# Optimization experiments

Hardware: AMD Instinct MI355X
Metric: run time of the kernel (lower is better)

Reference implementation:

```python
import jax, jax.numpy as jnp
import numpy as np
import itertools

B, T, D, H, E, K = 2, 1024, 768, 3072, 8, 2


def _trigram_dirs():
    # 8 vertices of the cube {-1,+1}^3, L2-normalized rows (matches F.normalize)
    t = np.array(list(itertools.product([-1.0, 1.0], repeat=3)), dtype=np.float32)[:E]
    t = t / np.linalg.norm(t, axis=1, keepdims=True)
    return jnp.asarray(t)


def setup_inputs() -> dict:
    key = jax.random.key(0)
    k1, k2, k3, k4 = jax.random.split(key, 4)
    x = jax.random.normal(k1, (B, T, D), jnp.float32)
    Wr = jax.random.normal(k2, (3, D), jnp.float32) * 0.02
    W1 = jax.random.normal(k3, (E, D, H), jnp.float32) * 0.02
    W2 = jax.random.normal(k4, (E, H, D), jnp.float32) * 0.02
    return {"x": x, "Wr": Wr, "W1": W1, "W2": W2}


def reference(x, Wr, W1, W2):
    Bb, Tt, Dd = x.shape
    xf = x.reshape(-1, Dd)                       # (N, D)
    dirs = _trigram_dirs()                       # (E, 3)
    z3 = xf @ Wr.T                               # (N, 3)
    logits = z3 @ dirs.T                         # (N, E)
    probs = jax.nn.softmax(logits, axis=-1)
    topv, topi = jax.lax.top_k(probs, K)         # (N, K)
    topv = topv / topv.sum(axis=-1, keepdims=True)
    N = xf.shape[0]
    # dense gate matrix: gates[n, e] = sum_k topv[n,k] * [topi[n,k]==e]
    gates = jnp.zeros((N, E), xf.dtype).at[jnp.arange(N)[:, None], topi].add(topv)
    # dense-all-experts equivalent of the masked gather/scatter loop
    h = jax.nn.gelu(jnp.einsum('nd,edh->neh', xf, W1), approximate=False)
    y = jnp.einsum('neh,ehd->ned', h, W2)
    out = jnp.einsum('ne,ned->nd', gates, y).reshape(Bb, Tt, Dd)
    tokens_per_expert = probs.mean(axis=0)
    aux_loss = 0.01 * jnp.mean((tokens_per_expert - 1.0 / E) ** 2)
    return out, aux_loss
```

## Files before the change

### kernel.cpp

```cpp
#include <hip/hip_runtime.h>
#include <hip/hip_bf16.h>
#include <math.h>

#define DD 768
#define HH 3072
#define EE 8
#define NN 2048
#define PP 5120
#define PT 40

typedef __attribute__((ext_vector_type(8))) short short8;
typedef __attribute__((ext_vector_type(4))) float floatx4;

typedef const __attribute__((address_space(1))) void gas_void;
typedef __attribute__((address_space(3))) void las_void;

__device__ __forceinline__ void gld16(const void* g, void* l) {
    __builtin_amdgcn_global_load_lds((gas_void*)g, (las_void*)l, 16, 0, 0);
}

__device__ __forceinline__ unsigned short f2bf(float f) {
    union { float f; unsigned int u; } v; v.f = f;
    unsigned int u = v.u;
    u += 0x7fffu + ((u >> 16) & 1u);
    return (unsigned short)(u >> 16);
}

__global__ __launch_bounds__(256) void routing_kernel(
    const float* __restrict__ x, const float* __restrict__ Wr,
    int* __restrict__ counts, float* __restrict__ psum,
    int* __restrict__ top_e, float* __restrict__ top_g)
{
    __shared__ float wr[3 * DD];
    __shared__ float lpsum[EE];
    int tid = threadIdx.x;
    for (int i = tid; i < 3 * DD; i += 256) wr[i] = Wr[i];
    if (tid < EE) lpsum[tid] = 0.f;
    __syncthreads();

    int sub = tid & 15;
    int n = blockIdx.x * 16 + (tid >> 4);
    const float* xr = x + (size_t)n * DD;
    float z0 = 0.f, z1 = 0.f, z2 = 0.f;
#pragma unroll
    for (int i = 0; i < DD / 64; i++) {
        int d = i * 64 + sub * 4;
        float4 v = *(const float4*)(xr + d);
        z0 = fmaf(v.x, wr[d], z0);         z0 = fmaf(v.y, wr[d+1], z0);
        z0 = fmaf(v.z, wr[d+2], z0);       z0 = fmaf(v.w, wr[d+3], z0);
        z1 = fmaf(v.x, wr[DD+d], z1);      z1 = fmaf(v.y, wr[DD+d+1], z1);
        z1 = fmaf(v.z, wr[DD+d+2], z1);    z1 = fmaf(v.w, wr[DD+d+3], z1);
        z2 = fmaf(v.x, wr[2*DD+d], z2);    z2 = fmaf(v.y, wr[2*DD+d+1], z2);
        z2 = fmaf(v.z, wr[2*DD+d+2], z2);  z2 = fmaf(v.w, wr[2*DD+d+3], z2);
    }
#pragma unroll
    for (int m = 8; m; m >>= 1) {
        z0 += __shfl_xor(z0, m, 16);
        z1 += __shfl_xor(z1, m, 16);
        z2 += __shfl_xor(z2, m, 16);
    }

    if (sub == 0) {
        const float r3 = 0.57735026918962576f;
        float p[EE];
        float mx = -1e30f;
#pragma unroll
        for (int e = 0; e < EE; e++) {
            float s0 = (e & 4) ? z0 : -z0;
            float s1 = (e & 2) ? z1 : -z1;
            float s2 = (e & 1) ? z2 : -z2;
            p[e] = (s0 + s1 + s2) * r3;
            mx = fmaxf(mx, p[e]);
        }
        float sum = 0.f;
#pragma unroll
        for (int e = 0; e < EE; e++) { p[e] = expf(p[e] - mx); sum += p[e]; }
        float inv_s = 1.f / sum;
#pragma unroll
        for (int e = 0; e < EE; e++) p[e] *= inv_s;

        int e1 = 0; float p1 = p[0];
#pragma unroll
        for (int e = 1; e < EE; e++) if (p[e] > p1) { p1 = p[e]; e1 = e; }
        int e2 = -1; float p2 = -1.f;
#pragma unroll
        for (int e = 0; e < EE; e++) if (e != e1 && p[e] > p2) { p2 = p[e]; e2 = e; }
        float inv_t = 1.f / (p1 + p2);
        top_e[2*n]   = e1;  top_g[2*n]   = p1 * inv_t;
        top_e[2*n+1] = e2;  top_g[2*n+1] = p2 * inv_t;
        atomicAdd(&counts[e1], 1);
        atomicAdd(&counts[e2], 1);
#pragma unroll
        for (int e = 0; e < EE; e++) atomicAdd(&lpsum[e], p[e]);
    }
    __syncthreads();
    if (tid < EE) atomicAdd(&psum[tid], lpsum[tid]);
}

__global__ void scan_aux_kernel(const int* __restrict__ counts, const float* __restrict__ psum,
                                int* __restrict__ cursor, int* __restrict__ poffs,
                                float* __restrict__ out_aux)
{
    if (threadIdx.x == 0) {
        int run = 0;
        for (int e = 0; e < EE; e++) {
            poffs[e] = run;
            cursor[e] = run;
            run += ((counts[e] + 127) >> 7) << 7;
        }
        poffs[EE] = run;
        float s = 0.f;
        for (int e = 0; e < EE; e++) {
            float t = psum[e] * (1.f / NN) - (1.f / EE);
            s += t * t;
        }
        *out_aux = 0.01f * (s * (1.f / EE));
    }
}

__global__ __launch_bounds__(256) void scatter_kernel(
    const int* __restrict__ top_e, int* __restrict__ cursor,
    int* __restrict__ row_tok, int* __restrict__ inv_row)
{
    int n = blockIdx.x * 256 + threadIdx.x;
#pragma unroll
    for (int k = 0; k < 2; k++) {
        int e = top_e[2*n + k];
        int pos = atomicAdd(&cursor[e], 1);
        row_tok[pos]    = n;
        inv_row[2*n+k]  = pos;
    }
}

__global__ __launch_bounds__(192) void gather_cast_kernel(
    const float* __restrict__ x, const int* __restrict__ counts,
    const int* __restrict__ poffs, const int* __restrict__ row_tok,
    unsigned short* __restrict__ xg)
{
    int t = threadIdx.x;
    int pr = blockIdx.x * 4 + t / 48;
    int c0 = (t % 48) * 16;
    int e = 0;
#pragma unroll
    for (int i = 0; i < EE - 1; i++) if (pr >= poffs[i + 1]) e = i + 1;
    int local = pr - poffs[e];
    unsigned short* dst = xg + (size_t)pr * DD + c0;
    if (local < counts[e]) {
        int tok = row_tok[pr];
        const float4* sp = (const float4*)(x + (size_t)tok * DD + c0);
        alignas(16) unsigned short tmp[16];
#pragma unroll
        for (int j = 0; j < 4; j++) {
            float4 v = sp[j];
            tmp[4*j+0] = f2bf(v.x); tmp[4*j+1] = f2bf(v.y);
            tmp[4*j+2] = f2bf(v.z); tmp[4*j+3] = f2bf(v.w);
        }
        *(uint4*)dst       = *(uint4*)&tmp[0];
        *(uint4*)(dst + 8) = *(uint4*)&tmp[8];
    } else {
        uint4 z = {0, 0, 0, 0};
        *(uint4*)dst       = z;
        *(uint4*)(dst + 8) = z;
    }
}

__global__ __launch_bounds__(256) void transpose_cast_kernel(
    const float* __restrict__ W1, const float* __restrict__ W2,
    unsigned short* __restrict__ w1t, unsigned short* __restrict__ w2t)
{
    int z = blockIdx.z, e = blockIdx.y, bx = blockIdx.x;
    const float* src; unsigned short* dst; int R, C, SC;
    if (z == 0) { R = DD; C = HH; SC = 12; src = W1 + (size_t)e * R * C; dst = w1t + (size_t)e * R * C; }
    else        { R = HH; C = DD; SC = 3;  src = W2 + (size_t)e * R * C; dst = w2t + (size_t)e * R * C; }
    int rt = bx / SC, cs = bx % SC;
    int r0 = rt * 64, cbase = cs * 256;

    __shared__ unsigned short tile[64][66];
    int tid = threadIdx.x;
    int lr = tid >> 2, lc = (tid & 3) * 16;
    int oc = tid >> 2, orr = (tid & 3) * 16;
    const float* srow = src + (size_t)(r0 + lr) * C + cbase + lc;

    float4 v[16];
#pragma unroll
    for (int i = 0; i < 4; i++) {
        const float4* sp = (const float4*)(srow + i * 64);
#pragma unroll
        for (int j = 0; j < 4; j++) v[i * 4 + j] = sp[j];
    }
#pragma unroll
    for (int i = 0; i < 16; i++)
        asm volatile("" :: "v"(v[i].x), "v"(v[i].y), "v"(v[i].z), "v"(v[i].w));

#pragma unroll
    for (int i = 0; i < 4; i++) {
        if (i) __syncthreads();
#pragma unroll
        for (int j = 0; j < 4; j++) {
            float4 t = v[i * 4 + j];
            tile[lr][lc + 4*j + 0] = f2bf(t.x);
            tile[lr][lc + 4*j + 1] = f2bf(t.y);
            tile[lr][lc + 4*j + 2] = f2bf(t.z);
            tile[lr][lc + 4*j + 3] = f2bf(t.w);
        }
        __syncthreads();
        alignas(16) unsigned short tmp[16];
#pragma unroll
        for (int j = 0; j < 16; j++) tmp[j] = tile[orr + j][oc];
        unsigned short* dp = dst + (size_t)(cbase + i * 64 + oc) * R + r0 + orr;
        *(uint4*)dp       = *(uint4*)&tmp[0];
        *(uint4*)(dp + 8) = *(uint4*)&tmp[8];
    }
}

__global__ __launch_bounds__(256) void gemm1_kernel(
    const unsigned short* __restrict__ xg, const unsigned short* __restrict__ w1t,
    unsigned short* __restrict__ h, const int* __restrict__ poffs)
{
    int t = blockIdx.x;
    if (t * 128 >= poffs[EE]) return;
    int e = 0;
#pragma unroll
    for (int i = 0; i < EE - 1; i++) if (t * 128 >= poffs[i + 1]) e = i + 1;
    int row0 = t * 128, n0 = blockIdx.y * 128;

    __shared__ alignas(16) unsigned short As[2][128][32];
    __shared__ alignas(16) unsigned short Bs[2][128][32];

    int tid = threadIdx.x;
    int w = tid >> 6, lane = tid & 63;
    int quad = lane >> 4, l15 = lane & 15;
    int wm = (w & 1) * 64, wn = (w >> 1) * 64;

    const unsigned short* abase = xg + (size_t)row0 * DD;
    const unsigned short* bbase = w1t + (size_t)e * HH * DD + (size_t)n0 * DD;

    int c0 = w * 64 + lane, c1 = 256 + c0;
    const unsigned short* ga0 = abase + (c0 >> 2) * DD + (c0 & 3) * 8;
    const unsigned short* ga1 = abase + (c1 >> 2) * DD + (c1 & 3) * 8;
    const unsigned short* gb0 = bbase + (c0 >> 2) * DD + (c0 & 3) * 8;
    const unsigned short* gb1 = bbase + (c1 >> 2) * DD + (c1 & 3) * 8;
    int lofs0 = (w * 64) * 8;
    int lofs1 = (256 + w * 64) * 8;

    floatx4 acc[4][4];
#pragma unroll
    for (int i = 0; i < 4; i++)
#pragma unroll
        for (int j = 0; j < 4; j++)
#pragma unroll
            for (int r = 0; r < 4; r++) acc[i][j][r] = 0.f;

    const int NT = DD / 32;
    gld16(ga0, &As[0][0][0] + lofs0);
    gld16(ga1, &As[0][0][0] + lofs1);
    gld16(gb0, &Bs[0][0][0] + lofs0);
    gld16(gb1, &Bs[0][0][0] + lofs1);
    __syncthreads();

    for (int kt = 0; kt < NT; kt++) {
        int cur = kt & 1;
        if (kt + 1 < NT) {
            int k0 = (kt + 1) * 32;
            unsigned short* nA = &As[cur ^ 1][0][0];
            unsigned short* nB = &Bs[cur ^ 1][0][0];
            gld16(ga0 + k0, nA + lofs0);
            gld16(ga1 + k0, nA + lofs1);
            gld16(gb0 + k0, nB + lofs0);
            gld16(gb1 + k0, nB + lofs1);
        }
        short8 afr[4], bfr[4];
#pragma unroll
        for (int fm = 0; fm < 4; fm++) afr[fm] = *(const short8*)&As[cur][wm + fm*16 + l15][quad * 8];
#pragma unroll
        for (int fn = 0; fn < 4; fn++) bfr[fn] = *(const short8*)&Bs[cur][wn + fn*16 + l15][quad * 8];
#pragma unroll
        for (int fm = 0; fm < 4; fm++)
#pragma unroll
            for (int fn = 0; fn < 4; fn++)
                acc[fm][fn] = __builtin_amdgcn_mfma_f32_16x16x32_bf16(afr[fm], bfr[fn], acc[fm][fn], 0, 0, 0);
        __syncthreads();
    }

#pragma unroll
    for (int fm = 0; fm < 4; fm++)
#pragma unroll
        for (int r = 0; r < 4; r++) {
            int rt = wm + fm * 16 + quad * 4 + r;
            size_t hrow = (size_t)(row0 + rt) * HH;
#pragma unroll
            for (int fn = 0; fn < 4; fn++) {
                int col = n0 + wn + fn * 16 + l15;
                float v = acc[fm][fn][r];
                float g = 0.5f * v * (1.f + erff(v * 0.70710678118654752f));
                h[hrow + col] = f2bf(g);
            }
        }
}

__global__ __launch_bounds__(256) void gemm2_kernel(
    const unsigned short* __restrict__ h, const unsigned short* __restrict__ w2t,
    float* __restrict__ ybuf, const int* __restrict__ poffs)
{
    int t = blockIdx.x;
    if (t * 128 >= poffs[EE]) return;
    int e = 0;
#pragma unroll
    for (int i = 0; i < EE - 1; i++) if (t * 128 >= poffs[i + 1]) e = i + 1;
    int row0 = t * 128, n0 = blockIdx.y * 128;
    int kz = blockIdx.z;

    __shared__ alignas(16) unsigned short As[2][128][32];
    __shared__ alignas(16) unsigned short Bs[2][128][32];

    int tid = threadIdx.x;
    int w = tid >> 6, lane = tid & 63;
    int quad = lane >> 4, l15 = lane & 15;
    int wm = (w & 1) * 64, wn = (w >> 1) * 64;

    const unsigned short* abase = h + (size_t)row0 * HH + kz * (HH / 2);
    const unsigned short* bbase = w2t + (size_t)e * DD * HH + (size_t)n0 * HH + kz * (HH / 2);

    int c0 = w * 64 + lane, c1 = 256 + c0;
    const unsigned short* ga0 = abase + (c0 >> 2) * HH + (c0 & 3) * 8;
    const unsigned short* ga1 = abase + (c1 >> 2) * HH + (c1 & 3) * 8;
    const unsigned short* gb0 = bbase + (c0 >> 2) * HH + (c0 & 3) * 8;
    const unsigned short* gb1 = bbase + (c1 >> 2) * HH + (c1 & 3) * 8;
    int lofs0 = (w * 64) * 8;
    int lofs1 = (256 + w * 64) * 8;

    floatx4 acc[4][4];
#pragma unroll
    for (int i = 0; i < 4; i++)
#pragma unroll
        for (int j = 0; j < 4; j++)
#pragma unroll
            for (int r = 0; r < 4; r++) acc[i][j][r] = 0.f;

    const int NT = (HH / 2) / 32;
    gld16(ga0, &As[0][0][0] + lofs0);
    gld16(ga1, &As[0][0][0] + lofs1);
    gld16(gb0, &Bs[0][0][0] + lofs0);
    gld16(gb1, &Bs[0][0][0] + lofs1);
    __syncthreads();

    for (int kt = 0; kt < NT; kt++) {
        int cur = kt & 1;
        if (kt + 1 < NT) {
            int k0 = (kt + 1) * 32;
            unsigned short* nA = &As[cur ^ 1][0][0];
            unsigned short* nB = &Bs[cur ^ 1][0][0];
            gld16(ga0 + k0, nA + lofs0);
            gld16(ga1 + k0, nA + lofs1);
            gld16(gb0 + k0, nB + lofs0);
            gld16(gb1 + k0, nB + lofs1);
        }
        short8 afr[4], bfr[4];
#pragma unroll
        for (int fm = 0; fm < 4; fm++) afr[fm] = *(const short8*)&As[cur][wm + fm*16 + l15][quad * 8];
#pragma unroll
        for (int fn = 0; fn < 4; fn++) bfr[fn] = *(const short8*)&Bs[cur][wn + fn*16 + l15][quad * 8];
#pragma unroll
        for (int fm = 0; fm < 4; fm++)
#pragma unroll
            for (int fn = 0; fn < 4; fn++)
                acc[fm][fn] = __builtin_amdgcn_mfma_f32_16x16x32_bf16(afr[fm], bfr[fn], acc[fm][fn], 0, 0, 0);
        __syncthreads();
    }

    float* yb = ybuf + (size_t)kz * PP * DD + (size_t)row0 * DD;
#pragma unroll
    for (int fm = 0; fm < 4; fm++)
#pragma unroll
        for (int r = 0; r < 4; r++) {
            int rt = wm + fm * 16 + quad * 4 + r;
            float* op = yb + (size_t)rt * DD + n0 + wn;
#pragma unroll
            for (int fn = 0; fn < 4; fn++)
                op[fn * 16 + l15] = acc[fm][fn][r];
        }
}

__global__ __launch_bounds__(192) void combine_kernel(
    const float* __restrict__ ybuf, const int* __restrict__ inv_row,
    const float* __restrict__ top_g, float* __restrict__ out)
{
    int n = blockIdx.x;
    int c = threadIdx.x * 4;
    int r0 = inv_row[2*n], r1 = inv_row[2*n+1];
    float g0 = top_g[2*n], g1 = top_g[2*n+1];
    const size_t S = (size_t)PP * DD;
    const float* y0 = ybuf + (size_t)r0 * DD + c;
    const float* y1 = ybuf + (size_t)r1 * DD + c;
    float4 a0 = *(const float4*)y0, b0 = *(const float4*)(y0 + S);
    float4 a1 = *(const float4*)y1, b1 = *(const float4*)(y1 + S);
    float4 o;
    o.x = g0 * (a0.x + b0.x) + g1 * (a1.x + b1.x);
    o.y = g0 * (a0.y + b0.y) + g1 * (a1.y + b1.y);
    o.z = g0 * (a0.z + b0.z) + g1 * (a1.z + b1.z);
    o.w = g0 * (a0.w + b0.w) + g1 * (a1.w + b1.w);
    *(float4*)(out + (size_t)n * DD + c) = o;
}

extern "C" void kernel_launch(void* const* d_in, const int* in_sizes, int n_in,
                              void* d_out, int out_size, void* d_ws, size_t ws_size,
                              hipStream_t stream)
{
    const float* x  = (const float*)d_in[0];
    const float* Wr = (const float*)d_in[1];
    const float* W1 = (const float*)d_in[2];
    const float* W2 = (const float*)d_in[3];
    float* out = (float*)d_out;

    char* ws = (char*)d_ws;
    int*   counts   = (int*)(ws + 0);
    int*   cursor   = (int*)(ws + 32);
    float* psum     = (float*)(ws + 64);
    int*   poffs    = (int*)(ws + 96);
    int*   top_e    = (int*)(ws + 1024);
    float* top_g    = (float*)(ws + 1024 + 16384);
    int*   row_tok  = (int*)(ws + 1024 + 2 * 16384);
    int*   inv_row  = (int*)(ws + 1024 + 2 * 16384 + PP * 4);
    size_t off = (size_t)(1024 + 2 * 16384 + PP * 4 + 16384 + 255) & ~(size_t)255;
    unsigned short* xg  = (unsigned short*)(ws + off); off += (size_t)PP * DD * 2;
    unsigned short* hbf = (unsigned short*)(ws + off); off += (size_t)PP * HH * 2;
    unsigned short* w1t = (unsigned short*)(ws + off); off += (size_t)EE * DD * HH * 2;
    unsigned short* w2t = (unsigned short*)(ws + off);
    float* ybuf = (float*)w1t;

    hipMemsetAsync(ws, 0, 96, stream);

    transpose_cast_kernel<<<dim3(144, EE, 2), 256, 0, stream>>>(W1, W2, w1t, w2t);
    routing_kernel<<<dim3(NN / 16), 256, 0, stream>>>(x, Wr, counts, psum, top_e, top_g);
    scan_aux_kernel<<<1, 64, 0, stream>>>(counts, psum, cursor, poffs, out + (size_t)NN * DD);
    scatter_kernel<<<dim3(NN / 256), 256, 0, stream>>>(top_e, cursor, row_tok, inv_row);
    gather_cast_kernel<<<dim3(PP / 4), 192, 0, stream>>>(x, counts, poffs, row_tok, xg);
    gemm1_kernel<<<dim3(PT, HH / 128), 256, 0, stream>>>(xg, w1t, hbf, poffs);
    gemm2_kernel<<<dim3(PT, DD / 128, 2), 256, 0, stream>>>(hbf, w2t, ybuf, poffs);
    combine_kernel<<<dim3(NN), 192, 0, stream>>>(ybuf, inv_row, top_g, out);
}
```

Before: 347.0 us.

## Triple-buffer LDS tiles with prefetch distance two in both expert GEMMs

```diff
diff --git a/kernel.cpp b/kernel.cpp
--- a/kernel.cpp
+++ b/kernel.cpp
@@ -224,8 +224,8 @@
     for (int i = 0; i < EE - 1; i++) if (t * 128 >= poffs[i + 1]) e = i + 1;
     int row0 = t * 128, n0 = blockIdx.y * 128;
 
-    __shared__ alignas(16) unsigned short As[2][128][32];
-    __shared__ alignas(16) unsigned short Bs[2][128][32];
+    __shared__ alignas(16) unsigned short As[3][128][32];
+    __shared__ alignas(16) unsigned short Bs[3][128][32];
 
     int tid = threadIdx.x;
     int w = tid >> 6, lane = tid & 63;
@@ -242,6 +242,8 @@
     const unsigned short* gb1 = bbase + (c1 >> 2) * DD + (c1 & 3) * 8;
     int lofs0 = (w * 64) * 8;
     int lofs1 = (256 + w * 64) * 8;
+    unsigned short* asb = &As[0][0][0];
+    unsigned short* bsb = &Bs[0][0][0];
 
     floatx4 acc[4][4];
 #pragma unroll
@@ -252,34 +254,39 @@
             for (int r = 0; r < 4; r++) acc[i][j][r] = 0.f;
 
     const int NT = DD / 32;
-    gld16(ga0, &As[0][0][0] + lofs0);
-    gld16(ga1, &As[0][0][0] + lofs1);
-    gld16(gb0, &Bs[0][0][0] + lofs0);
-    gld16(gb1, &Bs[0][0][0] + lofs1);
-    __syncthreads();
-
+    gld16(ga0,      asb + lofs0);  gld16(ga1,      asb + lofs1);
+    gld16(gb0,      bsb + lofs0);  gld16(gb1,      bsb + lofs1);
+    gld16(ga0 + 32, asb + 4096 + lofs0);  gld16(ga1 + 32, asb + 4096 + lofs1);
+    gld16(gb0 + 32, bsb + 4096 + lofs0);  gld16(gb1 + 32, bsb + 4096 + lofs1);
+    asm volatile("s_waitcnt vmcnt(4)" ::: "memory");
+    asm volatile("s_barrier" ::: "memory");
+
+    int cur = 0, pre = 2;
     for (int kt = 0; kt < NT; kt++) {
-        int cur = kt & 1;
-        if (kt + 1 < NT) {
-            int k0 = (kt + 1) * 32;
-            unsigned short* nA = &As[cur ^ 1][0][0];
-            unsigned short* nB = &Bs[cur ^ 1][0][0];
-            gld16(ga0 + k0, nA + lofs0);
-            gld16(ga1 + k0, nA + lofs1);
-            gld16(gb0 + k0, nB + lofs0);
-            gld16(gb1 + k0, nB + lofs1);
-        }
+        const unsigned short* A = asb + cur * 4096;
+        const unsigned short* B = bsb + cur * 4096;
         short8 afr[4], bfr[4];
 #pragma unroll
-        for (int fm = 0; fm < 4; fm++) afr[fm] = *(const short8*)&As[cur][wm + fm*16 + l15][quad * 8];
-#pragma unroll
-        for (int fn = 0; fn < 4; fn++) bfr[fn] = *(const short8*)&Bs[cur][wn + fn*16 + l15][quad * 8];
+        for (int fm = 0; fm < 4; fm++) afr[fm] = *(const short8*)(A + (wm + fm*16 + l15) * 32 + quad * 8);
+#pragma unroll
+        for (int fn = 0; fn < 4; fn++) bfr[fn] = *(const short8*)(B + (wn + fn*16 + l15) * 32 + quad * 8);
+        if (kt < NT - 2) {
+            int k0 = (kt + 2) * 32;
+            unsigned short* PA = asb + pre * 4096;
+            unsigned short* PB = bsb + pre * 4096;
+            gld16(ga0 + k0, PA + lofs0);  gld16(ga1 + k0, PA + lofs1);
+            gld16(gb0 + k0, PB + lofs0);  gld16(gb1 + k0, PB + lofs1);
+        }
 #pragma unroll
         for (int fm = 0; fm < 4; fm++)
 #pragma unroll
             for (int fn = 0; fn < 4; fn++)
                 acc[fm][fn] = __builtin_amdgcn_mfma_f32_16x16x32_bf16(afr[fm], bfr[fn], acc[fm][fn], 0, 0, 0);
-        __syncthreads();
+        if (kt < NT - 2) asm volatile("s_waitcnt vmcnt(4) lgkmcnt(0)" ::: "memory");
+        else             asm volatile("s_waitcnt vmcnt(0) lgkmcnt(0)" ::: "memory");
+        asm volatile("s_barrier" ::: "memory");
+        cur = (cur == 2) ? 0 : cur + 1;
+        pre = (pre == 2) ? 0 : pre + 1;
     }
 
 #pragma unroll
@@ -310,8 +317,8 @@
     int row0 = t * 128, n0 = blockIdx.y * 128;
     int kz = blockIdx.z;
 
-    __shared__ alignas(16) unsigned short As[2][128][32];
-    __shared__ alignas(16) unsigned short Bs[2][128][32];
+    __shared__ alignas(16) unsigned short As[3][128][32];
+    __shared__ alignas(16) unsigned short Bs[3][128][32];
 
     int tid = threadIdx.x;
     int w = tid >> 6, lane = tid & 63;
@@ -328,6 +335,8 @@
     const unsigned short* gb1 = bbase + (c1 >> 2) * HH + (c1 & 3) * 8;
     int lofs0 = (w * 64) * 8;
     int lofs1 = (256 + w * 64) * 8;
+    unsigned short* asb = &As[0][0][0];
+    unsigned short* bsb = &Bs[0][0][0];
 
     floatx4 acc[4][4];
 #pragma unroll
@@ -338,34 +347,39 @@
             for (int r = 0; r < 4; r++) acc[i][j][r] = 0.f;
 
     const int NT = (HH / 2) / 32;
-    gld16(ga0, &As[0][0][0] + lofs0);
-    gld16(ga1, &As[0][0][0] + lofs1);
-    gld16(gb0, &Bs[0][0][0] + lofs0);
-    gld16(gb1, &Bs[0][0][0] + lofs1);
-    __syncthreads();
-
+    gld16(ga0,      asb + lofs0);  gld16(ga1,      asb + lofs1);
+    gld16(gb0,      bsb + lofs0);  gld16(gb1,      bsb + lofs1);
+    gld16(ga0 + 32, asb + 4096 + lofs0);  gld16(ga1 + 32, asb + 4096 + lofs1);
+    gld16(gb0 + 32, bsb + 4096 + lofs0);  gld16(gb1 + 32, bsb + 4096 + lofs1);
+    asm volatile("s_waitcnt vmcnt(4)" ::: "memory");
+    asm volatile("s_barrier" ::: "memory");
+
+    int cur = 0, pre = 2;
     for (int kt = 0; kt < NT; kt++) {
-        int cur = kt & 1;
-        if (kt + 1 < NT) {
-            int k0 = (kt + 1) * 32;
-            unsigned short* nA = &As[cur ^ 1][0][0];
-            unsigned short* nB = &Bs[cur ^ 1][0][0];
-            gld16(ga0 + k0, nA + lofs0);
-            gld16(ga1 + k0, nA + lofs1);
-            gld16(gb0 + k0, nB + lofs0);
-            gld16(gb1 + k0, nB + lofs1);
-        }
+        const unsigned short* A = asb + cur * 4096;
+        const unsigned short* B = bsb + cur * 4096;
         short8 afr[4], bfr[4];
 #pragma unroll
-        for (int fm = 0; fm < 4; fm++) afr[fm] = *(const short8*)&As[cur][wm + fm*16 + l15][quad * 8];
-#pragma unroll
-        for (int fn = 0; fn < 4; fn++) bfr[fn] = *(const short8*)&Bs[cur][wn + fn*16 + l15][quad * 8];
+        for (int fm = 0; fm < 4; fm++) afr[fm] = *(const short8*)(A + (wm + fm*16 + l15) * 32 + quad * 8);
+#pragma unroll
+        for (int fn = 0; fn < 4; fn++) bfr[fn] = *(const short8*)(B + (wn + fn*16 + l15) * 32 + quad * 8);
+        if (kt < NT - 2) {
+            int k0 = (kt + 2) * 32;
+            unsigned short* PA = asb + pre * 4096;
+            unsigned short* PB = bsb + pre * 4096;
+            gld16(ga0 + k0, PA + lofs0);  gld16(ga1 + k0, PA + lofs1);
+            gld16(gb0 + k0, PB + lofs0);  gld16(gb1 + k0, PB + lofs1);
+        }
 #pragma unroll
         for (int fm = 0; fm < 4; fm++)
 #pragma unroll
             for (int fn = 0; fn < 4; fn++)
                 acc[fm][fn] = __builtin_amdgcn_mfma_f32_16x16x32_bf16(afr[fm], bfr[fn], acc[fm][fn], 0, 0, 0);
-        __syncthreads();
+        if (kt < NT - 2) asm volatile("s_waitcnt vmcnt(4) lgkmcnt(0)" ::: "memory");
+        else             asm volatile("s_waitcnt vmcnt(0) lgkmcnt(0)" ::: "memory");
+        asm volatile("s_barrier" ::: "memory");
+        cur = (cur == 2) ? 0 : cur + 1;
+        pre = (pre == 2) ? 0 : pre + 1;
     }
 
     float* yb = ybuf + (size_t)kz * PP * DD + (size_t)row0 * DD;
```

After: 335.1 us. 1.04x faster.
